# Performance work log

Hardware: AMD Instinct MI355X
Metric: run time of the kernel (lower is better)

The kernel has to match this reference:

```python
import jax, jax.numpy as jnp
import numpy as np

NUM_CLASSES = 21
NEGPOS_RATIO = 3
B, P = 64, 24564


def setup_inputs() -> dict:
    key = jax.random.key(0)
    ks = jax.random.split(key, 10)
    return {
        "loc_data": jax.random.normal(ks[0], (B, P, 4), jnp.float32),
        "conf_data": jax.random.normal(ks[1], (B, P, NUM_CLASSES), jnp.float32),
        "has_lp_data": jax.random.normal(ks[2], (B, P, 2), jnp.float32),
        "size_lp_data": jax.random.normal(ks[3], (B, P, 2), jnp.float32),
        "offset_data": jax.random.normal(ks[4], (B, P, 2), jnp.float32),
        "loc_t": jax.random.normal(ks[5], (B, P, 4), jnp.float32),
        "conf_t": jax.random.randint(ks[6], (B, P), 0, NUM_CLASSES, jnp.int64),
        "has_lp_t": jax.random.randint(ks[7], (B, P), 0, 2, jnp.int64),
        "size_lp_t": jax.random.normal(ks[8], (B, P, 2), jnp.float32),
        "offset_t": jax.random.normal(ks[9], (B, P, 2), jnp.float32),
    }


def _smooth_l1_sum(p, t, mask):
    # sum-reduced smooth L1 (beta=1) over elements selected by mask
    d = jnp.abs(p - t)
    l = jnp.where(d < 1.0, 0.5 * d * d, d - 0.5)
    return jnp.sum(l * mask)


def _ce_per_row(logits, labels):
    # per-row cross entropy: logsumexp(logits) - logits[label]
    lse = jax.nn.logsumexp(logits, axis=-1)
    g = jnp.take_along_axis(logits, labels[..., None], axis=-1)[..., 0]
    return lse - g


def reference(loc_data, conf_data, has_lp_data, size_lp_data, offset_data,
              loc_t, conf_t, has_lp_t, size_lp_t, offset_t):
    dt = loc_data.dtype
    num_priors = conf_data.shape[1]
    pos = conf_t > 0                                  # [B,P]
    posf = pos.astype(dt)[..., None]                  # [B,P,1]

    # localization loss over positives
    loss_l = _smooth_l1_sum(loc_data, loc_t, posf)

    # size / offset losses over positives, gated by has_lp flag
    hlp = has_lp_t.astype(dt)[..., None]              # [B,P,1]
    loss_size_lp = _smooth_l1_sum(size_lp_data * hlp, size_lp_t * hlp, posf)
    loss_offset = _smooth_l1_sum(offset_data * hlp, offset_t * hlp, posf)

    # hard negative mining on per-prior conf CE
    ce = _ce_per_row(conf_data, conf_t)               # [B,P]
    ce_mine = jnp.where(pos, 0.0, ce)
    loss_idx = jnp.argsort(-ce_mine, axis=1)          # descending sort indices
    idx_rank = jnp.argsort(loss_idx, axis=1)          # rank of each prior
    num_pos = jnp.sum(pos, axis=1, keepdims=True)     # [B,1]
    num_neg = jnp.clip(NEGPOS_RATIO * num_pos, None, num_priors - 1)
    neg = idx_rank < num_neg                          # [B,P]
    sel = (pos | neg).astype(dt)

    loss_c = jnp.sum(ce * sel)
    loss_has_lp = jnp.sum(_ce_per_row(has_lp_data, has_lp_t) * sel)

    N = jnp.sum(pos).astype(dt)
    return (loss_l / N, loss_c / N, loss_size_lp / N,
            loss_offset / N, loss_has_lp / N)
```

## Files before the change

kernel.cpp:

```cpp
#include <hip/hip_runtime.h>
#include <stdint.h>

#define NC 21
#define BATCH 64
#define PRI 24564
#define NROWS (BATCH * PRI)
#define SLABS 32
#define SLABR 768
#define GBLK (BATCH * SLABS)
#define BTHR 1024
#define BITER 24
#define NSTRIPE (BITER * 16)

typedef float f4a4 __attribute__((ext_vector_type(4), aligned(4)));

__device__ __forceinline__ float sl1f(float p, float t) {
    float d = fabsf(p - t);
    return d < 1.0f ? 0.5f * d * d : d - 0.5f;
}

__device__ __forceinline__ unsigned int f2k(float v) {
    unsigned int u = __float_as_uint(v);
    return (u & 0x80000000u) ? ~u : (u | 0x80000000u);
}

__device__ __forceinline__ double blockReduce(double v, double* sred) {
    #pragma unroll
    for (int off = 32; off > 0; off >>= 1)
        v += __shfl_down(v, off, 64);
    const int wid = threadIdx.x >> 6, lane = threadIdx.x & 63;
    __syncthreads();
    if (lane == 0) sred[wid] = v;
    __syncthreads();
    double r = 0.0;
    if (threadIdx.x == 0) r = sred[0] + sred[1] + sred[2] + sred[3];
    return r;
}

__device__ __forceinline__ double bred16(double v, double* sred) {
    #pragma unroll
    for (int off = 32; off > 0; off >>= 1)
        v += __shfl_down(v, off, 64);
    const int wid = threadIdx.x >> 6, lane = threadIdx.x & 63;
    __syncthreads();
    if (lane == 0) sred[wid] = v;
    __syncthreads();
    double r = 0.0;
    if (threadIdx.x == 0) {
        #pragma unroll
        for (int i = 0; i < 16; ++i) r += sred[i];
    }
    __syncthreads();
    return r;
}

__global__ __launch_bounds__(256, 4) void k_main(
    const float* __restrict__ loc_data, const float* __restrict__ conf_data,
    const float* __restrict__ has_lp_data, const float* __restrict__ size_lp_data,
    const float* __restrict__ offset_data, const float* __restrict__ loc_t,
    const int* __restrict__ conf_t, const int* __restrict__ has_lp_t,
    const float* __restrict__ size_lp_t, const float* __restrict__ offset_t,
    float2* __restrict__ ws_ch, double* __restrict__ part)
{
    __shared__ double sred[4];
    const int tid = threadIdx.x;
    const int b = blockIdx.x >> 5, s = blockIdx.x & 31;

    int pr[3]; bool vld[3];
    #pragma unroll
    for (int i = 0; i < 3; ++i) {
        int p = s * SLABR + i * 256 + tid;
        vld[i] = p < PRI;
        pr[i] = vld[i] ? p : PRI - 1;
    }
    const unsigned rb = (unsigned)b * PRI;

    int ct[3];
    #pragma unroll
    for (int i = 0; i < 3; ++i) ct[i] = conf_t[rb + pr[i]];
    f4a4 cw[3][5]; float c20[3], gg[3];
    #pragma unroll
    for (int i = 0; i < 3; ++i) {
        const float* crow = conf_data + (long)(rb + pr[i]) * NC;
        #pragma unroll
        for (int j = 0; j < 5; ++j) cw[i][j] = ((const f4a4*)crow)[j];
        c20[i] = crow[20];
        gg[i] = crow[ct[i]];
    }
    float ce[3];
    #pragma unroll
    for (int i = 0; i < 3; ++i) {
        float m = c20[i];
        #pragma unroll
        for (int j = 0; j < 5; ++j)
            m = fmaxf(m, fmaxf(fmaxf(cw[i][j].x, cw[i][j].y), fmaxf(cw[i][j].z, cw[i][j].w)));
        float sum = __expf(c20[i] - m);
        #pragma unroll
        for (int j = 0; j < 5; ++j)
            sum += __expf(cw[i][j].x - m) + __expf(cw[i][j].y - m)
                 + __expf(cw[i][j].z - m) + __expf(cw[i][j].w - m);
        ce[i] = m + __logf(sum) - gg[i];
    }

    int hl[3]; float4 lp[3], lt[3]; float2 sp2[3], st2[3], op2[3], ot2[3], hh[3];
    #pragma unroll
    for (int i = 0; i < 3; ++i) {
        const unsigned r = rb + pr[i];
        hl[i] = has_lp_t[r];
        lp[i] = ((const float4*)loc_data)[r];
        lt[i] = ((const float4*)loc_t)[r];
        sp2[i] = ((const float2*)size_lp_data)[r];
        st2[i] = ((const float2*)size_lp_t)[r];
        op2[i] = ((const float2*)offset_data)[r];
        ot2[i] = ((const float2*)offset_t)[r];
        hh[i] = ((const float2*)has_lp_data)[r];
    }
    double aL = 0.0, aS = 0.0, aO = 0.0;
    int myp = 0, myn = 0;
    #pragma unroll
    for (int i = 0; i < 3; ++i) {
        const bool pos = ct[i] > 0;
        float ll = sl1f(lp[i].x, lt[i].x) + sl1f(lp[i].y, lt[i].y)
                 + sl1f(lp[i].z, lt[i].z) + sl1f(lp[i].w, lt[i].w);
        float ls = sl1f(sp2[i].x, st2[i].x) + sl1f(sp2[i].y, st2[i].y);
        float lo = sl1f(op2[i].x, ot2[i].x) + sl1f(op2[i].y, ot2[i].y);
        const float pf = (vld[i] && pos) ? 1.f : 0.f;
        const float hf = (hl[i] != 0) ? 1.f : 0.f;
        aL += (double)(pf * ll);
        aS += (double)(pf * hf * ls);
        aO += (double)(pf * hf * lo);
        float hm = fmaxf(hh[i].x, hh[i].y);
        float hs = __expf(hh[i].x - hm) + __expf(hh[i].y - hm);
        float hlce = fmaxf(hm + __logf(hs) - (hl[i] != 0 ? hh[i].y : hh[i].x), 0.0f);
        unsigned hb = __float_as_uint(hlce) | (pos ? 0x80000000u : 0u);
        if (vld[i]) ws_ch[rb + pr[i]] = make_float2(ce[i], __uint_as_float(hb));
        myp += (vld[i] && pos) ? 1 : 0;
        myn += (vld[i] && !pos && f2k(ce[i]) != 0x80000000u) ? 1 : 0;
    }

    double v;
    v = blockReduce(aL, sred); if (tid == 0) part[0 * GBLK + blockIdx.x] = v;
    v = blockReduce(aS, sred); if (tid == 0) part[1 * GBLK + blockIdx.x] = v;
    v = blockReduce(aO, sred); if (tid == 0) part[2 * GBLK + blockIdx.x] = v;
    v = blockReduce((double)myp, sred);
    if (tid == 0) part[3 * GBLK + blockIdx.x] = v;
    v = blockReduce((double)myn, sred);
    if (tid == 0) part[4 * GBLK + blockIdx.x] = v;
}

__global__ __launch_bounds__(BTHR) void k_batch(
    const float2* __restrict__ ws_ch, const double* __restrict__ part,
    double* __restrict__ lossCH)
{
    const int b = blockIdx.x, tid = threadIdx.x;
    const int lane = tid & 63, wid = tid >> 6;
    __shared__ int shist[4096];
    __shared__ int sct[BTHR];
    __shared__ int sCnt[NSTRIPE];
    __shared__ double sTC[NSTRIPE], sTH[NSTRIPE];
    __shared__ double sred[16];
    __shared__ double s_np, s_M;
    __shared__ unsigned s_dig;
    __shared__ int s_rem;
    __shared__ int s_st, s_loc;

    const float2* row = ws_ch + (unsigned)b * PRI;

    if (wid == 0) {
        double np = 0.0, mm = 0.0;
        if (lane < 32) {
            np = part[3 * GBLK + b * 32 + lane];
            mm = part[4 * GBLK + b * 32 + lane];
        }
        #pragma unroll
        for (int off = 32; off > 0; off >>= 1) {
            np += __shfl_down(np, off, 64);
            mm += __shfl_down(mm, off, 64);
        }
        if (lane == 0) { s_np = np; s_M = mm; }
    }
    __syncthreads();
    int K = 3 * (int)(s_np + 0.5);
    if (K > PRI - 1) K = PRI - 1;
    const int M = (int)(s_M + 0.5);

    if (K <= 0) {
        if (tid == 0) { lossCH[b] = 0.0; lossCH[64 + b] = 0.0; }
        return;
    }

    unsigned T; int need;
    if (K > M) {
        T = 0x80000000u; need = K - M;
    } else {
        for (int k = tid; k < 4096; k += BTHR) shist[k] = 0;
        __syncthreads();
        for (int i = 0; i < BITER; ++i) {
            const int p = i * BTHR + tid;
            if (p < PRI) {
                float2 ch = row[p];
                unsigned hb = __float_as_uint(ch.y);
                if (!(hb >> 31)) {
                    unsigned key = f2k(ch.x);
                    if (key != 0x80000000u) atomicAdd(&shist[key >> 20], 1);
                }
            }
        }
        __syncthreads();
        {
            int h4[4]; int ctn = 0;
            #pragma unroll
            for (int j = 0; j < 4; ++j) { h4[j] = shist[tid * 4 + j]; ctn += h4[j]; }
            sct[tid] = ctn;
            __syncthreads();
            #pragma unroll
            for (int off = 1; off < BTHR; off <<= 1) {
                int v = (tid + off < BTHR) ? sct[tid + off] : 0;
                __syncthreads();
                sct[tid] += v;
                __syncthreads();
            }
            const int Sa = (tid < BTHR - 1) ? sct[tid + 1] : 0;
            int cum = Sa;
            #pragma unroll
            for (int j = 3; j >= 0; --j) {
                int c2 = cum + h4[j];
                if (c2 >= K && cum < K) { s_dig = (unsigned)(tid * 4 + j); s_rem = K - cum; }
                cum = c2;
            }
            __syncthreads();
        }
        unsigned pref = s_dig; int rem = s_rem;
        __syncthreads();

        if (tid < 1024) shist[tid] = 0;
        __syncthreads();
        for (int i = 0; i < BITER; ++i) {
            const int p = i * BTHR + tid;
            if (p < PRI) {
                float2 ch = row[p];
                unsigned hb = __float_as_uint(ch.y);
                if (!(hb >> 31)) {
                    unsigned key = f2k(ch.x);
                    if (key != 0x80000000u && (key >> 20) == pref)
                        atomicAdd(&shist[(key >> 10) & 1023], 1);
                }
            }
        }
        __syncthreads();
        {
            const int hb1 = shist[tid];
            sct[tid] = hb1;
            __syncthreads();
            #pragma unroll
            for (int off = 1; off < BTHR; off <<= 1) {
                int v = (tid + off < BTHR) ? sct[tid + off] : 0;
                __syncthreads();
                sct[tid] += v;
                __syncthreads();
            }
            const int Sa = (tid < BTHR - 1) ? sct[tid + 1] : 0;
            if (Sa + hb1 >= rem && Sa < rem) { s_dig = (unsigned)tid; s_rem = rem - Sa; }
            __syncthreads();
        }
        pref = (pref << 10) | s_dig; rem = s_rem;
        __syncthreads();

        if (tid < 1024) shist[tid] = 0;
        __syncthreads();
        for (int i = 0; i < BITER; ++i) {
            const int p = i * BTHR + tid;
            if (p < PRI) {
                float2 ch = row[p];
                unsigned hb = __float_as_uint(ch.y);
                if (!(hb >> 31)) {
                    unsigned key = f2k(ch.x);
                    if (key != 0x80000000u && (key >> 10) == pref)
                        atomicAdd(&shist[key & 1023], 1);
                }
            }
        }
        __syncthreads();
        {
            const int hb1 = shist[tid];
            sct[tid] = hb1;
            __syncthreads();
            #pragma unroll
            for (int off = 1; off < BTHR; off <<= 1) {
                int v = (tid + off < BTHR) ? sct[tid + off] : 0;
                __syncthreads();
                sct[tid] += v;
                __syncthreads();
            }
            const int Sa = (tid < BTHR - 1) ? sct[tid + 1] : 0;
            if (Sa + hb1 >= rem && Sa < rem) { s_dig = (unsigned)tid; s_rem = rem - Sa; }
            __syncthreads();
        }
        T = (pref << 10) | s_dig; need = s_rem;
        __syncthreads();
    }

    double aC = 0.0, aH = 0.0;
    for (int i = 0; i < BITER; ++i) {
        const int p = i * BTHR + tid;
        const bool valid = p < PRI;
        float2 ch = valid ? row[p] : make_float2(0.f, 0.f);
        const unsigned hb = __float_as_uint(ch.y);
        const bool pos = (hb >> 31) != 0;
        const unsigned key = pos ? 0x80000000u : f2k(ch.x);
        const float hlv = __uint_as_float(hb & 0x7fffffffu);
        if (valid && (pos || key > T)) { aC += (double)ch.x; aH += (double)hlv; }
        const bool eq = valid && (key == T);
        const unsigned long long msk = __ballot(eq);
        double tc = (eq && !pos) ? (double)ch.x : 0.0;
        double th = (eq && !pos) ? (double)hlv : 0.0;
        #pragma unroll
        for (int off = 32; off > 0; off >>= 1) {
            tc += __shfl_down(tc, off, 64);
            th += __shfl_down(th, off, 64);
        }
        if (lane == 0) {
            sCnt[i * 16 + wid] = (int)__popcll(msk);
            sTC[i * 16 + wid] = tc;
            sTH[i * 16 + wid] = th;
        }
    }
    const double aCt = bred16(aC, sred);
    const double aHt = bred16(aH, sred);

    double accC = 0.0, accH = 0.0;
    if (tid == 0) {
        int st = -1, loc = 0, cum = 0;
        if (need > 0) {
            for (int s2 = 0; s2 < NSTRIPE; ++s2) {
                const int c = sCnt[s2];
                if (cum + c >= need) { st = s2; loc = need - cum; break; }
                cum += c;
                accC += sTC[s2]; accH += sTH[s2];
            }
        }
        s_st = st; s_loc = loc;
    }
    __syncthreads();
    const int st = s_st, loc = s_loc;

    double pC = 0.0, pH = 0.0;
    if (wid == 0 && st >= 0) {
        const int base = (st >> 4) * BTHR + (st & 15) * 64;
        const int p = base + lane;
        const bool valid = p < PRI;
        float2 ch = valid ? row[p] : make_float2(0.f, 0.f);
        const unsigned hb = __float_as_uint(ch.y);
        const bool pos = (hb >> 31) != 0;
        const unsigned key = pos ? 0x80000000u : f2k(ch.x);
        const float hlv = __uint_as_float(hb & 0x7fffffffu);
        const bool eq = valid && (key == T);
        const unsigned long long msk = __ballot(eq);
        const int rank = (int)__popcll(msk & ((1ull << lane) - 1ull)) + 1;
        int sel = (eq && rank == loc) ? lane : 64;
        #pragma unroll
        for (int off = 32; off > 0; off >>= 1) {
            int o = __shfl_xor(sel, off, 64);
            sel = (o < sel) ? o : sel;
        }
        const bool take = eq && !pos && (lane <= sel);
        pC = take ? (double)ch.x : 0.0;
        pH = take ? (double)hlv : 0.0;
        #pragma unroll
        for (int off = 32; off > 0; off >>= 1) {
            pC += __shfl_down(pC, off, 64);
            pH += __shfl_down(pH, off, 64);
        }
    }
    if (tid == 0) {
        lossCH[b] = aCt + accC + pC;
        lossCH[64 + b] = aHt + accH + pH;
    }
}

__global__ __launch_bounds__(256) void k_final(
    const double* __restrict__ part, const double* __restrict__ lossCH,
    float* __restrict__ out)
{
    __shared__ double sred[4];
    const int tid = threadIdx.x;
    double s[3];
    #pragma unroll
    for (int k = 0; k < 3; ++k) {
        double a = 0.0;
        for (int t = tid; t < GBLK; t += 256) a += part[k * GBLK + t];
        s[k] = blockReduce(a, sred);
    }
    double a = 0.0;
    for (int t = tid; t < GBLK; t += 256) a += part[3 * GBLK + t];
    double n = blockReduce(a, sred);
    double lc = (tid < BATCH) ? lossCH[tid] : 0.0;
    lc = blockReduce(lc, sred);
    double lh = (tid < BATCH) ? lossCH[64 + tid] : 0.0;
    lh = blockReduce(lh, sred);
    if (tid == 0) {
        out[0] = (float)(s[0] / n);
        out[1] = (float)(lc / n);
        out[2] = (float)(s[1] / n);
        out[3] = (float)(s[2] / n);
        out[4] = (float)(lh / n);
    }
}

extern "C" void kernel_launch(void* const* d_in, const int* in_sizes, int n_in,
                              void* d_out, int out_size, void* d_ws, size_t ws_size,
                              hipStream_t stream)
{
    const float* loc_data     = (const float*)d_in[0];
    const float* conf_data    = (const float*)d_in[1];
    const float* has_lp_data  = (const float*)d_in[2];
    const float* size_lp_data = (const float*)d_in[3];
    const float* offset_data  = (const float*)d_in[4];
    const float* loc_t        = (const float*)d_in[5];
    const int*   conf_t       = (const int*)d_in[6];
    const int*   has_lp_t    = (const int*)d_in[7];
    const float* size_lp_t    = (const float*)d_in[8];
    const float* offset_t     = (const float*)d_in[9];
    float* out = (float*)d_out;

    char* ws = (char*)d_ws;
    double* part     = (double*)(ws + 16384);
    double* lossCH   = (double*)(ws + 131072);
    float2* ws_ch    = (float2*)(ws + 1704960);

    k_main<<<GBLK, 256, 0, stream>>>(loc_data, conf_data, has_lp_data, size_lp_data,
                                     offset_data, loc_t, conf_t, has_lp_t,
                                     size_lp_t, offset_t, ws_ch, part);
    k_batch<<<BATCH, BTHR, 0, stream>>>(ws_ch, part, lossCH);
    k_final<<<1, 256, 0, stream>>>(part, lossCH, out);
}
```

Measured before the change: 388.6 us.

## Stage conf logits through shared memory with coalesced loads, one row per thread

The main kernel now gives each block 256 priors of one batch row, one prior per thread, on a 2D grid. Each block first copies its conf_data tile into LDS with fully coalesced scalar loads, then each thread reads its 21 logits from LDS. The odd stride of 21 keeps those LDS reads free of bank conflicts. Before, each thread issued strided, unaligned vector loads straight from global memory. The change adds a __syncthreads and about 21 KB of LDS per block, and it triples the number of partial sums that k_batch and k_final must reduce.

```diff
diff --git a/kernel.cpp b/kernel.cpp
--- a/kernel.cpp
+++ b/kernel.cpp
@@ -5,14 +5,11 @@
 #define BATCH 64
 #define PRI 24564
 #define NROWS (BATCH * PRI)
-#define SLABS 32
-#define SLABR 768
-#define GBLK (BATCH * SLABS)
+#define NBJ 96
+#define NB (BATCH * NBJ)
 #define BTHR 1024
 #define BITER 24
 #define NSTRIPE (BITER * 16)
-
-typedef float f4a4 __attribute__((ext_vector_type(4), aligned(4)));
 
 __device__ __forceinline__ float sl1f(float p, float t) {
     float d = fabsf(p - t);
@@ -62,90 +59,78 @@
     const float* __restrict__ size_lp_t, const float* __restrict__ offset_t,
     float2* __restrict__ ws_ch, double* __restrict__ part)
 {
+    __shared__ float sconf[256 * NC];
     __shared__ double sred[4];
     const int tid = threadIdx.x;
-    const int b = blockIdx.x >> 5, s = blockIdx.x & 31;
-
-    int pr[3]; bool vld[3];
-    #pragma unroll
-    for (int i = 0; i < 3; ++i) {
-        int p = s * SLABR + i * 256 + tid;
-        vld[i] = p < PRI;
-        pr[i] = vld[i] ? p : PRI - 1;
-    }
+    const int b = blockIdx.y, j = blockIdx.x;
+    const int r0 = j * 256;
+    const int vrows = (PRI - r0 < 256) ? (PRI - r0) : 256;
     const unsigned rb = (unsigned)b * PRI;
 
-    int ct[3];
-    #pragma unroll
-    for (int i = 0; i < 3; ++i) ct[i] = conf_t[rb + pr[i]];
-    f4a4 cw[3][5]; float c20[3], gg[3];
-    #pragma unroll
-    for (int i = 0; i < 3; ++i) {
-        const float* crow = conf_data + (long)(rb + pr[i]) * NC;
+    const bool vld = tid < vrows;
+    const int p = vld ? (r0 + tid) : (PRI - 1);
+    const unsigned r = rb + p;
+
+    const int ct = conf_t[r];
+    const int hl = has_lp_t[r];
+    const float4 lp = ((const float4*)loc_data)[r];
+    const float4 lt = ((const float4*)loc_t)[r];
+    const float2 sp2 = ((const float2*)size_lp_data)[r];
+    const float2 st2 = ((const float2*)size_lp_t)[r];
+    const float2 op2 = ((const float2*)offset_data)[r];
+    const float2 ot2 = ((const float2*)offset_t)[r];
+    const float2 hh = ((const float2*)has_lp_data)[r];
+
+    {
+        const float* src = conf_data + (long)(rb + r0) * NC;
+        const int nfl = vrows * NC;
         #pragma unroll
-        for (int j = 0; j < 5; ++j) cw[i][j] = ((const f4a4*)crow)[j];
-        c20[i] = crow[20];
-        gg[i] = crow[ct[i]];
-    }
-    float ce[3];
-    #pragma unroll
-    for (int i = 0; i < 3; ++i) {
-        float m = c20[i];
-        #pragma unroll
-        for (int j = 0; j < 5; ++j)
-            m = fmaxf(m, fmaxf(fmaxf(cw[i][j].x, cw[i][j].y), fmaxf(cw[i][j].z, cw[i][j].w)));
-        float sum = __expf(c20[i] - m);
-        #pragma unroll
-        for (int j = 0; j < 5; ++j)
-            sum += __expf(cw[i][j].x - m) + __expf(cw[i][j].y - m)
-                 + __expf(cw[i][j].z - m) + __expf(cw[i][j].w - m);
-        ce[i] = m + __logf(sum) - gg[i];
-    }
-
-    int hl[3]; float4 lp[3], lt[3]; float2 sp2[3], st2[3], op2[3], ot2[3], hh[3];
-    #pragma unroll
-    for (int i = 0; i < 3; ++i) {
-        const unsigned r = rb + pr[i];
-        hl[i] = has_lp_t[r];
-        lp[i] = ((const float4*)loc_data)[r];
-        lt[i] = ((const float4*)loc_t)[r];
-        sp2[i] = ((const float2*)size_lp_data)[r];
-        st2[i] = ((const float2*)size_lp_t)[r];
-        op2[i] = ((const float2*)offset_data)[r];
-        ot2[i] = ((const float2*)offset_t)[r];
-        hh[i] = ((const float2*)has_lp_data)[r];
-    }
-    double aL = 0.0, aS = 0.0, aO = 0.0;
-    int myp = 0, myn = 0;
-    #pragma unroll
-    for (int i = 0; i < 3; ++i) {
-        const bool pos = ct[i] > 0;
-        float ll = sl1f(lp[i].x, lt[i].x) + sl1f(lp[i].y, lt[i].y)
-                 + sl1f(lp[i].z, lt[i].z) + sl1f(lp[i].w, lt[i].w);
-        float ls = sl1f(sp2[i].x, st2[i].x) + sl1f(sp2[i].y, st2[i].y);
-        float lo = sl1f(op2[i].x, ot2[i].x) + sl1f(op2[i].y, ot2[i].y);
-        const float pf = (vld[i] && pos) ? 1.f : 0.f;
-        const float hf = (hl[i] != 0) ? 1.f : 0.f;
-        aL += (double)(pf * ll);
-        aS += (double)(pf * hf * ls);
-        aO += (double)(pf * hf * lo);
-        float hm = fmaxf(hh[i].x, hh[i].y);
-        float hs = __expf(hh[i].x - hm) + __expf(hh[i].y - hm);
-        float hlce = fmaxf(hm + __logf(hs) - (hl[i] != 0 ? hh[i].y : hh[i].x), 0.0f);
-        unsigned hb = __float_as_uint(hlce) | (pos ? 0x80000000u : 0u);
-        if (vld[i]) ws_ch[rb + pr[i]] = make_float2(ce[i], __uint_as_float(hb));
-        myp += (vld[i] && pos) ? 1 : 0;
-        myn += (vld[i] && !pos && f2k(ce[i]) != 0x80000000u) ? 1 : 0;
-    }
-
+        for (int k = 0; k < NC; ++k) {
+            const int idx = k * 256 + tid;
+            if (idx < nfl) sconf[idx] = src[idx];
+        }
+    }
+    __syncthreads();
+
+    const float* cr = sconf + tid * NC;
+    float c[NC];
+    #pragma unroll
+    for (int q = 0; q < NC; ++q) c[q] = cr[q];
+    const float gg = cr[ct];
+    float m = c[0];
+    #pragma unroll
+    for (int q = 1; q < NC; ++q) m = fmaxf(m, c[q]);
+    float sum = 0.f;
+    #pragma unroll
+    for (int q = 0; q < NC; ++q) sum += __expf(c[q] - m);
+    const float ce = m + __logf(sum) - gg;
+
+    const bool pos = ct > 0;
+    float ll = sl1f(lp.x, lt.x) + sl1f(lp.y, lt.y) + sl1f(lp.z, lt.z) + sl1f(lp.w, lt.w);
+    float ls = sl1f(sp2.x, st2.x) + sl1f(sp2.y, st2.y);
+    float lo = sl1f(op2.x, ot2.x) + sl1f(op2.y, ot2.y);
+    const float pf = (vld && pos) ? 1.f : 0.f;
+    const float hf = (hl != 0) ? 1.f : 0.f;
+    const double aL = (double)(pf * ll);
+    const double aS = (double)(pf * hf * ls);
+    const double aO = (double)(pf * hf * lo);
+    const float hm = fmaxf(hh.x, hh.y);
+    const float hs = __expf(hh.x - hm) + __expf(hh.y - hm);
+    const float hlce = fmaxf(hm + __logf(hs) - (hl != 0 ? hh.y : hh.x), 0.0f);
+    const unsigned hb = __float_as_uint(hlce) | (pos ? 0x80000000u : 0u);
+    if (vld) ws_ch[r] = make_float2(ce, __uint_as_float(hb));
+    const int myp = (vld && pos) ? 1 : 0;
+    const int myn = (vld && !pos && f2k(ce) != 0x80000000u) ? 1 : 0;
+
+    const int sb = b * NBJ + j;
     double v;
-    v = blockReduce(aL, sred); if (tid == 0) part[0 * GBLK + blockIdx.x] = v;
-    v = blockReduce(aS, sred); if (tid == 0) part[1 * GBLK + blockIdx.x] = v;
-    v = blockReduce(aO, sred); if (tid == 0) part[2 * GBLK + blockIdx.x] = v;
+    v = blockReduce(aL, sred); if (tid == 0) part[0 * NB + sb] = v;
+    v = blockReduce(aS, sred); if (tid == 0) part[1 * NB + sb] = v;
+    v = blockReduce(aO, sred); if (tid == 0) part[2 * NB + sb] = v;
     v = blockReduce((double)myp, sred);
-    if (tid == 0) part[3 * GBLK + blockIdx.x] = v;
+    if (tid == 0) part[3 * NB + sb] = v;
     v = blockReduce((double)myn, sred);
-    if (tid == 0) part[4 * GBLK + blockIdx.x] = v;
+    if (tid == 0) part[4 * NB + sb] = v;
 }
 
 __global__ __launch_bounds__(BTHR) void k_batch(
@@ -166,18 +151,11 @@
 
     const float2* row = ws_ch + (unsigned)b * PRI;
 
-    if (wid == 0) {
-        double np = 0.0, mm = 0.0;
-        if (lane < 32) {
-            np = part[3 * GBLK + b * 32 + lane];
-            mm = part[4 * GBLK + b * 32 + lane];
-        }
-        #pragma unroll
-        for (int off = 32; off > 0; off >>= 1) {
-            np += __shfl_down(np, off, 64);
-            mm += __shfl_down(mm, off, 64);
-        }
-        if (lane == 0) { s_np = np; s_M = mm; }
+    {
+        double npv = bred16((tid < NBJ) ? part[3 * NB + b * NBJ + tid] : 0.0, sred);
+        if (tid == 0) s_np = npv;
+        double mmv = bred16((tid < NBJ) ? part[4 * NB + b * NBJ + tid] : 0.0, sred);
+        if (tid == 0) s_M = mmv;
     }
     __syncthreads();
     int K = 3 * (int)(s_np + 0.5);
@@ -388,11 +366,11 @@
     #pragma unroll
     for (int k = 0; k < 3; ++k) {
         double a = 0.0;
-        for (int t = tid; t < GBLK; t += 256) a += part[k * GBLK + t];
+        for (int t = tid; t < NB; t += 256) a += part[k * NB + t];
         s[k] = blockReduce(a, sred);
     }
     double a = 0.0;
-    for (int t = tid; t < GBLK; t += 256) a += part[3 * GBLK + t];
+    for (int t = tid; t < NB; t += 256) a += part[3 * NB + t];
     double n = blockReduce(a, sred);
     double lc = (tid < BATCH) ? lossCH[tid] : 0.0;
     lc = blockReduce(lc, sred);
@@ -418,19 +396,20 @@
     const float* offset_data  = (const float*)d_in[4];
     const float* loc_t        = (const float*)d_in[5];
     const int*   conf_t       = (const int*)d_in[6];
-    const int*   has_lp_t    = (const int*)d_in[7];
+    const int*   has_lp_t     = (const int*)d_in[7];
     const float* size_lp_t    = (const float*)d_in[8];
     const float* offset_t     = (const float*)d_in[9];
     float* out = (float*)d_out;
 
     char* ws = (char*)d_ws;
     double* part     = (double*)(ws + 16384);
-    double* lossCH   = (double*)(ws + 131072);
+    double* lossCH   = (double*)(ws + 262144);
     float2* ws_ch    = (float2*)(ws + 1704960);
 
-    k_main<<<GBLK, 256, 0, stream>>>(loc_data, conf_data, has_lp_data, size_lp_data,
-                                     offset_data, loc_t, conf_t, has_lp_t,
-                                     size_lp_t, offset_t, ws_ch, part);
+    k_main<<<dim3(NBJ, BATCH), 256, 0, stream>>>(loc_data, conf_data, has_lp_data,
+                                                 size_lp_data, offset_data, loc_t,
+                                                 conf_t, has_lp_t, size_lp_t, offset_t,
+                                                 ws_ch, part);
     k_batch<<<BATCH, BTHR, 0, stream>>>(ws_ch, part, lossCH);
     k_final<<<1, 256, 0, stream>>>(part, lossCH, out);
 }
```

New measurement: 419.9 us. 8.1% more time.

## Split main pass into separate CE and smooth-L1 kernels writing interleaved workspace

Applied to the files above, without the earlier changes.

Splits the fused per-prior kernel into two kernels. One computes conf cross-entropy and the pos/neg counts, the other computes the smooth-L1 and has_lp losses. Each writes its half of the interleaved float2 workspace. This lowers register pressure per kernel, at the cost of reading conf_t twice, making strided 4-byte stores instead of 8-byte ones, and adding one launch. It also changes k_batch to skip the tie-sum shuffles when no negative ties exist in a wave, and moves the count reduction onto the 16-wave block reduce.

```diff
diff --git a/kernel.cpp b/kernel.cpp
--- a/kernel.cpp
+++ b/kernel.cpp
@@ -54,13 +54,10 @@
     return r;
 }
 
-__global__ __launch_bounds__(256, 4) void k_main(
-    const float* __restrict__ loc_data, const float* __restrict__ conf_data,
-    const float* __restrict__ has_lp_data, const float* __restrict__ size_lp_data,
-    const float* __restrict__ offset_data, const float* __restrict__ loc_t,
-    const int* __restrict__ conf_t, const int* __restrict__ has_lp_t,
-    const float* __restrict__ size_lp_t, const float* __restrict__ offset_t,
-    float2* __restrict__ ws_ch, double* __restrict__ part)
+
+__global__ __launch_bounds__(256, 4) void k_ce(
+    const float* __restrict__ conf_data, const int* __restrict__ conf_t,
+    float* __restrict__ wsf , double* __restrict__ part)
 {
     __shared__ double sred[4];
     const int tid = threadIdx.x;
@@ -87,7 +84,7 @@
         c20[i] = crow[20];
         gg[i] = crow[ct[i]];
     }
-    float ce[3];
+    int myp = 0, myn = 0;
     #pragma unroll
     for (int i = 0; i < 3; ++i) {
         float m = c20[i];
@@ -99,13 +96,45 @@
         for (int j = 0; j < 5; ++j)
             sum += __expf(cw[i][j].x - m) + __expf(cw[i][j].y - m)
                  + __expf(cw[i][j].z - m) + __expf(cw[i][j].w - m);
-        ce[i] = m + __logf(sum) - gg[i];
-    }
-
-    int hl[3]; float4 lp[3], lt[3]; float2 sp2[3], st2[3], op2[3], ot2[3], hh[3];
+        const float ce = m + __logf(sum) - gg[i];
+        if (vld[i]) wsf[2u * (rb + pr[i])] = ce;
+        const bool pos = ct[i] > 0;
+        myp += (vld[i] && pos) ? 1 : 0;
+        myn += (vld[i] && !pos && f2k(ce) != 0x80000000u) ? 1 : 0;
+    }
+    double v;
+    v = blockReduce((double)myp, sred);
+    if (tid == 0) part[3 * GBLK + blockIdx.x] = v;
+    v = blockReduce((double)myn, sred);
+    if (tid == 0) part[4 * GBLK + blockIdx.x] = v;
+}
+
+__global__ __launch_bounds__(256, 4) void k_sl1(
+    const float* __restrict__ loc_data, const float* __restrict__ has_lp_data,
+    const float* __restrict__ size_lp_data, const float* __restrict__ offset_data,
+    const float* __restrict__ loc_t, const int* __restrict__ conf_t,
+    const int* __restrict__ has_lp_t, const float* __restrict__ size_lp_t,
+    const float* __restrict__ offset_t,
+    float* __restrict__ wsf , double* __restrict__ part)
+{
+    __shared__ double sred[4];
+    const int tid = threadIdx.x;
+    const int b = blockIdx.x >> 5, s = blockIdx.x & 31;
+
+    int pr[3]; bool vld[3];
+    #pragma unroll
+    for (int i = 0; i < 3; ++i) {
+        int p = s * SLABR + i * 256 + tid;
+        vld[i] = p < PRI;
+        pr[i] = vld[i] ? p : PRI - 1;
+    }
+    const unsigned rb = (unsigned)b * PRI;
+
+    int ct[3], hl[3]; float4 lp[3], lt[3]; float2 sp2[3], st2[3], op2[3], ot2[3], hh[3];
     #pragma unroll
     for (int i = 0; i < 3; ++i) {
         const unsigned r = rb + pr[i];
+        ct[i] = conf_t[r];
         hl[i] = has_lp_t[r];
         lp[i] = ((const float4*)loc_data)[r];
         lt[i] = ((const float4*)loc_t)[r];
@@ -116,7 +145,6 @@
         hh[i] = ((const float2*)has_lp_data)[r];
     }
     double aL = 0.0, aS = 0.0, aO = 0.0;
-    int myp = 0, myn = 0;
     #pragma unroll
     for (int i = 0; i < 3; ++i) {
         const bool pos = ct[i] > 0;
@@ -133,19 +161,12 @@
         float hs = __expf(hh[i].x - hm) + __expf(hh[i].y - hm);
         float hlce = fmaxf(hm + __logf(hs) - (hl[i] != 0 ? hh[i].y : hh[i].x), 0.0f);
         unsigned hb = __float_as_uint(hlce) | (pos ? 0x80000000u : 0u);
-        if (vld[i]) ws_ch[rb + pr[i]] = make_float2(ce[i], __uint_as_float(hb));
-        myp += (vld[i] && pos) ? 1 : 0;
-        myn += (vld[i] && !pos && f2k(ce[i]) != 0x80000000u) ? 1 : 0;
-    }
-
+        if (vld[i]) wsf[2u * (rb + pr[i]) + 1u] = __uint_as_float(hb);
+    }
     double v;
     v = blockReduce(aL, sred); if (tid == 0) part[0 * GBLK + blockIdx.x] = v;
     v = blockReduce(aS, sred); if (tid == 0) part[1 * GBLK + blockIdx.x] = v;
     v = blockReduce(aO, sred); if (tid == 0) part[2 * GBLK + blockIdx.x] = v;
-    v = blockReduce((double)myp, sred);
-    if (tid == 0) part[3 * GBLK + blockIdx.x] = v;
-    v = blockReduce((double)myn, sred);
-    if (tid == 0) part[4 * GBLK + blockIdx.x] = v;
 }
 
 __global__ __launch_bounds__(BTHR) void k_batch(
@@ -166,18 +187,11 @@
 
     const float2* row = ws_ch + (unsigned)b * PRI;
 
-    if (wid == 0) {
-        double np = 0.0, mm = 0.0;
-        if (lane < 32) {
-            np = part[3 * GBLK + b * 32 + lane];
-            mm = part[4 * GBLK + b * 32 + lane];
-        }
-        #pragma unroll
-        for (int off = 32; off > 0; off >>= 1) {
-            np += __shfl_down(np, off, 64);
-            mm += __shfl_down(mm, off, 64);
-        }
-        if (lane == 0) { s_np = np; s_M = mm; }
+    {
+        double npv = bred16((tid < SLABS) ? part[3 * GBLK + b * SLABS + tid] : 0.0, sred);
+        if (tid == 0) s_np = npv;
+        double mmv = bred16((tid < SLABS) ? part[4 * GBLK + b * SLABS + tid] : 0.0, sred);
+        if (tid == 0) s_M = mmv;
     }
     __syncthreads();
     int K = 3 * (int)(s_np + 0.5);
@@ -312,12 +326,16 @@
         if (valid && (pos || key > T)) { aC += (double)ch.x; aH += (double)hlv; }
         const bool eq = valid && (key == T);
         const unsigned long long msk = __ballot(eq);
-        double tc = (eq && !pos) ? (double)ch.x : 0.0;
-        double th = (eq && !pos) ? (double)hlv : 0.0;
-        #pragma unroll
-        for (int off = 32; off > 0; off >>= 1) {
-            tc += __shfl_down(tc, off, 64);
-            th += __shfl_down(th, off, 64);
+        const unsigned long long mneg = __ballot(eq && !pos);
+        double tc = 0.0, th = 0.0;
+        if (mneg) {
+            tc = (eq && !pos) ? (double)ch.x : 0.0;
+            th = (eq && !pos) ? (double)hlv : 0.0;
+            #pragma unroll
+            for (int off = 32; off > 0; off >>= 1) {
+                tc += __shfl_down(tc, off, 64);
+                th += __shfl_down(th, off, 64);
+            }
         }
         if (lane == 0) {
             sCnt[i * 16 + wid] = (int)__popcll(msk);
@@ -418,7 +436,7 @@
     const float* offset_data  = (const float*)d_in[4];
     const float* loc_t        = (const float*)d_in[5];
     const int*   conf_t       = (const int*)d_in[6];
-    const int*   has_lp_t    = (const int*)d_in[7];
+    const int*   has_lp_t     = (const int*)d_in[7];
     const float* size_lp_t    = (const float*)d_in[8];
     const float* offset_t     = (const float*)d_in[9];
     float* out = (float*)d_out;
@@ -427,10 +445,12 @@
     double* part     = (double*)(ws + 16384);
     double* lossCH   = (double*)(ws + 131072);
     float2* ws_ch    = (float2*)(ws + 1704960);
-
-    k_main<<<GBLK, 256, 0, stream>>>(loc_data, conf_data, has_lp_data, size_lp_data,
-                                     offset_data, loc_t, conf_t, has_lp_t,
-                                     size_lp_t, offset_t, ws_ch, part);
+    float*  wsf      = (float*)ws_ch;
+
+    k_ce<<<GBLK, 256, 0, stream>>>(conf_data, conf_t, wsf, part);
+    k_sl1<<<GBLK, 256, 0, stream>>>(loc_data, has_lp_data, size_lp_data, offset_data,
+                                    loc_t, conf_t, has_lp_t, size_lp_t, offset_t,
+                                    wsf, part);
     k_batch<<<BATCH, BTHR, 0, stream>>>(ws_ch, part, lossCH);
     k_final<<<1, 256, 0, stream>>>(part, lossCH, out);
 }
```

Result: faster. 374.7 us (-3.6%).
